# Kernel optimization log

Measured on AMD Instinct MI355X. Metric: run time of the kernel, lower is better.

The kernel has to match this reference:

```python
import jax, jax.numpy as jnp
import numpy as np

N_SAMPLES = 262144  # 2^18
DIM = 3
NUM_FLOWS = 8
HIDDEN = 64


def setup_inputs() -> dict:
    key = jax.random.key(0)
    ks = jax.random.split(key, 16)
    s = 0.05  # small param scale so exp() chains across 8 flows stay stable
    eps = jax.random.normal(ks[0], (N_SAMPLES, DIM), dtype=jnp.float32)
    L_tril = jnp.eye(DIM, dtype=jnp.float32) * np.float32(np.sqrt(0.1)) + s * jnp.tril(jax.random.normal(ks[1], (DIM, DIM), dtype=jnp.float32))
    base_mean = s * jax.random.normal(ks[2], (DIM,), dtype=jnp.float32)
    an_log_scale = s * jax.random.normal(ks[3], (NUM_FLOWS, DIM), dtype=jnp.float32)
    an_shift = s * jax.random.normal(ks[4], (NUM_FLOWS, DIM), dtype=jnp.float32)
    # permutation matrices (buffers, non-trainable)
    rng = np.random.RandomState(0)
    perm_p = np.zeros((NUM_FLOWS, DIM, DIM), dtype=np.float32)
    for i in range(NUM_FLOWS):
        perm = rng.permutation(DIM)
        perm_p[i, np.arange(DIM), perm] = 1.0
    perm_p = jnp.asarray(perm_p)
    sign_s = jnp.sign(jax.random.normal(ks[5], (NUM_FLOWS, DIM))) .astype(jnp.float32)
    sign_s = jnp.where(sign_s == 0, 1.0, sign_s)
    lu_l = s * jax.random.normal(ks[6], (NUM_FLOWS, DIM, DIM), dtype=jnp.float32)
    lu_u = s * jax.random.normal(ks[7], (NUM_FLOWS, DIM, DIM), dtype=jnp.float32)
    lu_log_s = s * jax.random.normal(ks[8], (NUM_FLOWS, DIM), dtype=jnp.float32)
    W1 = s * jax.random.normal(ks[9], (NUM_FLOWS, HIDDEN, 1), dtype=jnp.float32)
    b1 = s * jax.random.normal(ks[10], (NUM_FLOWS, HIDDEN), dtype=jnp.float32)
    W2 = s * jax.random.normal(ks[11], (NUM_FLOWS, HIDDEN, HIDDEN), dtype=jnp.float32)
    b2 = s * jax.random.normal(ks[12], (NUM_FLOWS, HIDDEN), dtype=jnp.float32)
    W3 = s * jax.random.normal(ks[13], (NUM_FLOWS, 4, HIDDEN), dtype=jnp.float32)
    b3 = s * jax.random.normal(ks[14], (NUM_FLOWS, 4), dtype=jnp.float32)
    return dict(eps=eps, L_tril=L_tril, base_mean=base_mean,
                an_log_scale=an_log_scale, an_shift=an_shift,
                perm_p=perm_p, sign_s=sign_s, lu_l=lu_l, lu_u=lu_u,
                lu_log_s=lu_log_s, W1=W1, b1=b1, W2=W2, b2=b2, W3=W3, b3=b3)


def _glow_forward(eps, L_tril, base_mean, an_log_scale, an_shift, perm_p,
                  sign_s, lu_l, lu_u, lu_log_s, W1, b1, W2, b2, W3, b3):
    eye = jnp.eye(DIM, dtype=eps.dtype)
    # base sample via Cholesky of (tril(L)+1e-6*I)(.)^T
    Lt = jnp.tril(L_tril) + eye * 1e-6
    cov = Lt @ Lt.T
    L = jnp.linalg.cholesky(cov)
    z = base_mean + eps @ L.T                      # [N, 3]
    log_det = jnp.zeros(eps.shape[0], dtype=eps.dtype)

    def step(carry, p):
        z, ld = carry
        ls, sh, P, ss, lm, um, lls, w1, bb1, w2, bb2, w3, bb3 = p
        # ActNorm
        z = jnp.exp(ls) * (z + sh)
        ld = ld + jnp.sum(ls)
        # Invertible 1x1 conv (LU parameterization)
        l = jnp.tril(lm, -1) + eye
        u = jnp.triu(um, 1)
        W = P @ l @ (u + jnp.diag(ss * jnp.exp(lls)))
        z = z @ W.T
        ld = ld + jnp.sum(lls)  # == slogdet(W)[1] since |det P|=1, det L=1
        # Affine coupling: split 1 / 2, MLP 1->64->64->4
        z1, z2 = z[:, :1], z[:, 1:]
        h = jax.nn.relu(z1 @ w1.T + bb1)
        h = jax.nn.relu(h @ w2.T + bb2)
        out = h @ w3.T + bb3                        # [N, 4]
        shift, log_scale = out[:, :2], out[:, 2:]
        z2 = z2 * jnp.exp(log_scale) + shift
        ld = ld + jnp.sum(log_scale, axis=1)
        return (jnp.concatenate([z1, z2], axis=1), ld), None

    (z, log_det), _ = jax.lax.scan(
        step, (z, log_det),
        (an_log_scale, an_shift, perm_p, sign_s, lu_l, lu_u, lu_log_s,
         W1, b1, W2, b2, W3, b3))

    # final positivity transform on columns 1, 2
    z_t = jnp.concatenate([z[:, :1], jnp.exp(z[:, 1:3])], axis=1)
    log_det = log_det + z[:, 1] + z[:, 2]
    return z_t, log_det


def reference(eps, L_tril, base_mean, an_log_scale, an_shift, perm_p, sign_s,
              lu_l, lu_u, lu_log_s, W1, b1, W2, b2, W3, b3):
    return _glow_forward(eps, L_tril, base_mean, an_log_scale, an_shift,
                         perm_p, sign_s, lu_l, lu_u, lu_log_s,
                         W1, b1, W2, b2, W3, b3)
```

## Files before the change

kernel.cpp:

```cpp
#include <hip/hip_runtime.h>
#include <hip/hip_bf16.h>

#define N_SAMPLES 262144
#define NUM_FLOWS 8
#define BLOCK 256
#define WAVES 4
#define MT 2
#define SAMPLES_PER_BLOCK (WAVES * MT * 16)
#define NBLOCKS (N_SAMPLES / SAMPLES_PER_BLOCK)

#define OFF_W1    0
#define OFF_B1    512
#define OFF_B2    1024
#define OFF_B3    1536
#define OFF_CONST 1568
#define OFF_LC    1696
#define OFF_MEAN  1708
#define OFF_LDB   1711
#define OFF_A3    1728
#define WS_PARAMS 5824
#define WS_W2_BYTE_OFF (WS_PARAMS * 4)
#define SP_FLOATS 1536

typedef __attribute__((ext_vector_type(8))) short bf16x8;
typedef __attribute__((ext_vector_type(4))) short shortx4;
typedef __attribute__((ext_vector_type(4))) float floatx4;

union FragU { bf16x8 v; __hip_bfloat162 p[4]; __hip_bfloat16 e[8]; };
union S4U   { shortx4 v; __hip_bfloat16 e[4]; };

__device__ __forceinline__ float b2f(__hip_bfloat16 x) { return __bfloat162float(x); }

__device__ __forceinline__ float ldv(const void* p, int i, bool f32) {
    return f32 ? ((const float*)p)[i] : b2f(((const __hip_bfloat16*)p)[i]);
}
__device__ __forceinline__ void stv(void* p, int i, float v, bool f32) {
    if (f32) ((float*)p)[i] = v;
    else ((__hip_bfloat16*)p)[i] = __float2bfloat16(v);
}

__global__ void prep_kernel(
    const void* __restrict__ g_L_tril,
    const void* __restrict__ g_base_mean,
    const void* __restrict__ g_an_log_scale,
    const void* __restrict__ g_an_shift,
    const void* __restrict__ g_perm_p,
    const void* __restrict__ g_sign_s,
    const void* __restrict__ g_lu_l,
    const void* __restrict__ g_lu_u,
    const void* __restrict__ g_lu_log_s,
    const void* __restrict__ g_W1,
    const void* __restrict__ g_b1,
    const void* __restrict__ g_W2,
    const void* __restrict__ g_b2,
    const void* __restrict__ g_W3,
    const void* __restrict__ g_b3,
    float* __restrict__ ws)
{
    const bool f32 = (((const float*)g_L_tril)[1] == 0.0f);
    const int f = blockIdx.x;
    const int tid = threadIdx.x;
    __hip_bfloat16* wsW2 = (__hip_bfloat16*)((char*)ws + WS_W2_BYTE_OFF);
    __hip_bfloat16* wsA3 = (__hip_bfloat16*)(ws + OFF_A3);

    if (f < NUM_FLOWS) {
        for (int i4 = tid; i4 < 1024; i4 += BLOCK) {
            int e = i4 << 2;
            int n = e >> 6, k = e & 63;
            int dst = ((k >> 5) * 4 + (n >> 4)) * 512 + (((k >> 3) & 3) * 16 + (n & 15)) * 8 + (k & 7);
            S4U u;
            if (f32) {
                float4 v = ((const float4*)g_W2)[f * 1024 + i4];
                u.e[0] = __float2bfloat16(v.x);
                u.e[1] = __float2bfloat16(v.y);
                u.e[2] = __float2bfloat16(v.z);
                u.e[3] = __float2bfloat16(v.w);
            } else {
                u.v = ((const shortx4*)g_W2)[f * 1024 + i4];
            }
            *(shortx4*)&wsW2[f * 4096 + dst] = u.v;
        }
        if (tid < 128) {
            int kc2 = tid >> 6, L = tid & 63;
            int m = L & 15, qd = L >> 4;
            FragU fr;
#pragma unroll
            for (int j = 0; j < 8; ++j) {
                int jt = ((j >> 2) << 1) | kc2;
                int r  = j & 3;
                int n  = jt * 16 + qd * 4 + r;
                fr.e[j] = __float2bfloat16(ldv(g_W3, f * 256 + (m & 3) * 64 + n, f32));
            }
            *(bf16x8*)&wsA3[(f * 2 + kc2) * 512 + L * 8] = fr.v;
        }
        if (tid < 64) {
            ws[OFF_W1 + f * 64 + tid] = ldv(g_W1, f * 64 + tid, f32);
            ws[OFF_B1 + f * 64 + tid] = ldv(g_b1, f * 64 + tid, f32);
            ws[OFF_B2 + f * 64 + tid] = ldv(g_b2, f * 64 + tid, f32);
        }
        if (tid < 4) ws[OFF_B3 + f * 4 + tid] = ldv(g_b3, f * 4 + tid, f32);
        if (tid == 0) {
            for (int d = 0; d < 3; ++d) {
                float ls = ldv(g_an_log_scale, f * 3 + d, f32);
                ws[OFF_CONST + f * 16 + 9 + d]  = __expf(ls);
                ws[OFF_CONST + f * 16 + 12 + d] = ldv(g_an_shift, f * 3 + d, f32);
            }
            float U[3][3], Lm[3][3], M[3][3], P[3][3];
            for (int i = 0; i < 3; ++i)
                for (int j = 0; j < 3; ++j) {
                    U[i][j]  = (j > i) ? ldv(g_lu_u, f * 9 + i * 3 + j, f32) : 0.f;
                    Lm[i][j] = (j < i) ? ldv(g_lu_l, f * 9 + i * 3 + j, f32) : (i == j ? 1.f : 0.f);
                    P[i][j]  = ldv(g_perm_p, f * 9 + i * 3 + j, f32);
                }
            for (int i = 0; i < 3; ++i)
                U[i][i] = ldv(g_sign_s, f * 3 + i, f32) * __expf(ldv(g_lu_log_s, f * 3 + i, f32));
            for (int i = 0; i < 3; ++i)
                for (int j = 0; j < 3; ++j) {
                    float s = 0.f;
                    for (int k = 0; k < 3; ++k) s += Lm[i][k] * U[k][j];
                    M[i][j] = s;
                }
            for (int i = 0; i < 3; ++i)
                for (int j = 0; j < 3; ++j) {
                    float s = 0.f;
                    for (int k = 0; k < 3; ++k) s += P[i][k] * M[k][j];
                    ws[OFF_CONST + f * 16 + i * 3 + j] = s;
                }
            ws[OFF_CONST + f * 16 + 15] = 0.f;
        }
    } else if (tid == 0) {
        float Lt[3][3];
        for (int i = 0; i < 3; ++i)
            for (int j = 0; j < 3; ++j)
                Lt[i][j] = (j <= i) ? ldv(g_L_tril, i * 3 + j, f32) : 0.f;
        for (int i = 0; i < 3; ++i) Lt[i][i] += 1e-6f;
        float cov[3][3];
        for (int i = 0; i < 3; ++i)
            for (int j = 0; j < 3; ++j) {
                float s = 0.f;
                for (int k = 0; k < 3; ++k) s += Lt[i][k] * Lt[j][k];
                cov[i][j] = s;
            }
        float c00 = sqrtf(cov[0][0]);
        float c10 = cov[1][0] / c00, c20 = cov[2][0] / c00;
        float c11 = sqrtf(cov[1][1] - c10 * c10);
        float c21 = (cov[2][1] - c20 * c10) / c11;
        float c22 = sqrtf(cov[2][2] - c20 * c20 - c21 * c21);
        ws[OFF_LC + 0] = c00; ws[OFF_LC + 3] = c10; ws[OFF_LC + 4] = c11;
        ws[OFF_LC + 6] = c20; ws[OFF_LC + 7] = c21; ws[OFF_LC + 8] = c22;
        ws[OFF_LC + 1] = 0.f; ws[OFF_LC + 2] = 0.f; ws[OFF_LC + 5] = 0.f;
        ws[OFF_LC + 9] = 0.f; ws[OFF_LC + 10] = 0.f; ws[OFF_LC + 11] = 0.f;
        for (int d = 0; d < 3; ++d) ws[OFF_MEAN + d] = ldv(g_base_mean, d, f32);
        float ldb = 0.f;
        for (int i = 0; i < NUM_FLOWS * 3; ++i)
            ldb += ldv(g_an_log_scale, i, f32) + ldv(g_lu_log_s, i, f32);
        ws[OFF_LDB] = ldb;
    }
}

__global__ __launch_bounds__(BLOCK, 2) void glow_kernel(
    const void* __restrict__ g_eps,
    const void* __restrict__ g_L_tril,
    const float* __restrict__ ws,
    void* __restrict__ g_out)
{
    const bool f32 = (((const float*)g_L_tril)[1] == 0.0f);

    __shared__ __align__(16) float sP[SP_FLOATS];
    for (int i = threadIdx.x; i < SP_FLOATS / 4; i += BLOCK)
        ((float4*)sP)[i] = ((const float4*)ws)[i];
    __syncthreads();

    const __hip_bfloat16* wsW2 = (const __hip_bfloat16*)((const char*)ws + WS_W2_BYTE_OFF);
    const __hip_bfloat16* wsA3 = (const __hip_bfloat16*)(ws + OFF_A3);

    const int tid  = threadIdx.x;
    const int lane = tid & 63;
    const int wave = tid >> 6;
    const int quad = lane >> 4;
    const int col  = lane & 15;
    const int base = blockIdx.x * SAMPLES_PER_BLOCK + wave * (MT * 16);

    float zc0[MT], zc1[MT], zc2[MT], lda[MT];
    {
        const float l00 = ws[OFF_LC + 0], l10 = ws[OFF_LC + 3], l11 = ws[OFF_LC + 4];
        const float l20 = ws[OFF_LC + 6], l21 = ws[OFF_LC + 7], l22 = ws[OFF_LC + 8];
        const float m0 = ws[OFF_MEAN], m1 = ws[OFF_MEAN + 1], m2 = ws[OFF_MEAN + 2];
#pragma unroll
        for (int mt = 0; mt < MT; ++mt) {
            int g = base + mt * 16 + col;
            float e0 = ldv(g_eps, g * 3 + 0, f32);
            float e1 = ldv(g_eps, g * 3 + 1, f32);
            float e2 = ldv(g_eps, g * 3 + 2, f32);
            zc0[mt] = m0 + l00 * e0;
            zc1[mt] = m1 + l10 * e0 + l11 * e1;
            zc2[mt] = m2 + l20 * e0 + l21 * e1 + l22 * e2;
            lda[mt] = 0.f;
        }
    }

#pragma unroll 1
    for (int f = 0; f < NUM_FLOWS; ++f) {
        bf16x8 Af[2][4];
#pragma unroll
        for (int kc = 0; kc < 2; ++kc)
#pragma unroll
            for (int jt = 0; jt < 4; ++jt)
                Af[kc][jt] = *(const bf16x8*)&wsW2[f * 4096 + ((kc * 4 + jt) * 64 + lane) * 8];
        bf16x8 A3f[2];
#pragma unroll
        for (int kc2 = 0; kc2 < 2; ++kc2)
            A3f[kc2] = *(const bf16x8*)&wsA3[((f * 2 + kc2) * 64 + lane) * 8];

        floatx4 b2q[4];
#pragma unroll
        for (int jt = 0; jt < 4; ++jt)
            b2q[jt] = *(const floatx4*)&sP[OFF_B2 + f * 64 + jt * 16 + quad * 4];

        const floatx4* cp = (const floatx4*)&ws[OFF_CONST + f * 16];
        floatx4 c0 = cp[0], c1 = cp[1], c2 = cp[2], c3 = cp[3];
        floatx4 b3v = *(const floatx4*)&ws[OFF_B3 + f * 4];

#pragma unroll
        for (int mt = 0; mt < MT; ++mt) {
            float t0 = c2[1] * (zc0[mt] + c3[0]);
            float t1 = c2[2] * (zc1[mt] + c3[1]);
            float t2 = c2[3] * (zc2[mt] + c3[2]);
            zc0[mt] = c0[0] * t0 + c0[1] * t1 + c0[2] * t2;
            zc1[mt] = c0[3] * t0 + c1[0] * t1 + c1[1] * t2;
            zc2[mt] = c1[2] * t0 + c1[3] * t1 + c2[0] * t2;
        }

        FragU hB[MT][2];
#pragma unroll
        for (int kc = 0; kc < 2; ++kc) {
            const floatx4* w1p = (const floatx4*)&sP[OFF_W1 + f * 64 + kc * 32 + quad * 8];
            const floatx4* b1p = (const floatx4*)&sP[OFF_B1 + f * 64 + kc * 32 + quad * 8];
            floatx4 w1a = w1p[0], w1b = w1p[1];
            floatx4 b1a = b1p[0], b1b = b1p[1];
#pragma unroll
            for (int mt = 0; mt < MT; ++mt) {
                float z0 = zc0[mt];
#pragma unroll
                for (int w = 0; w < 2; ++w) {
                    float a0 = fmaxf(fmaf(z0, w1a[2 * w],     b1a[2 * w]),     0.f);
                    float a1 = fmaxf(fmaf(z0, w1a[2 * w + 1], b1a[2 * w + 1]), 0.f);
                    float b0 = fmaxf(fmaf(z0, w1b[2 * w],     b1b[2 * w]),     0.f);
                    float b1 = fmaxf(fmaf(z0, w1b[2 * w + 1], b1b[2 * w + 1]), 0.f);
                    hB[mt][kc].p[w]     = __float22bfloat162_rn(make_float2(a0, a1));
                    hB[mt][kc].p[2 + w] = __float22bfloat162_rn(make_float2(b0, b1));
                }
            }
        }

#pragma unroll
        for (int mt = 0; mt < MT; ++mt) {
            floatx4 a2[4];
#pragma unroll
            for (int jt = 0; jt < 4; ++jt) {
                floatx4 acc = __builtin_amdgcn_mfma_f32_16x16x32_bf16(Af[0][jt], hB[mt][0].v, b2q[jt], 0, 0, 0);
                a2[jt] = __builtin_amdgcn_mfma_f32_16x16x32_bf16(Af[1][jt], hB[mt][1].v, acc, 0, 0, 0);
            }
            FragU h3[2];
#pragma unroll
            for (int jt = 0; jt < 4; ++jt) {
                int kc2 = jt & 1, pb = (jt >> 1) * 2;
                h3[kc2].p[pb]     = __float22bfloat162_rn(make_float2(fmaxf(a2[jt][0], 0.f), fmaxf(a2[jt][1], 0.f)));
                h3[kc2].p[pb + 1] = __float22bfloat162_rn(make_float2(fmaxf(a2[jt][2], 0.f), fmaxf(a2[jt][3], 0.f)));
            }
            floatx4 acc3 = {0.f, 0.f, 0.f, 0.f};
            acc3 = __builtin_amdgcn_mfma_f32_16x16x32_bf16(A3f[0], h3[0].v, acc3, 0, 0, 0);
            acc3 = __builtin_amdgcn_mfma_f32_16x16x32_bf16(A3f[1], h3[1].v, acc3, 0, 0, 0);
            float sh0 = acc3[0] + b3v[0];
            float sh1 = acc3[1] + b3v[1];
            float ls0 = acc3[2] + b3v[2];
            float ls1 = acc3[3] + b3v[3];
            zc1[mt] = fmaf(zc1[mt], __expf(ls0), sh0);
            zc2[mt] = fmaf(zc2[mt], __expf(ls1), sh1);
            lda[mt] += ls0 + ls1;
        }
    }

    if (quad == 0) {
        const float ldBase = ws[OFF_LDB];
#pragma unroll
        for (int mt = 0; mt < MT; ++mt) {
            int g = base + mt * 16 + col;
            float z1 = zc1[mt], z2 = zc2[mt];
            stv(g_out, g * 3 + 0, zc0[mt], f32);
            stv(g_out, g * 3 + 1, __expf(z1), f32);
            stv(g_out, g * 3 + 2, __expf(z2), f32);
            stv(g_out, 3 * N_SAMPLES + g, lda[mt] + ldBase + z1 + z2, f32);
        }
    }
}

extern "C" void kernel_launch(void* const* d_in, const int* in_sizes, int n_in,
                              void* d_out, int out_size, void* d_ws, size_t ws_size,
                              hipStream_t stream) {
    prep_kernel<<<dim3(NUM_FLOWS + 1), dim3(BLOCK), 0, stream>>>(
        d_in[1], d_in[2], d_in[3], d_in[4], d_in[5], d_in[6], d_in[7],
        d_in[8], d_in[9], d_in[10], d_in[11], d_in[12], d_in[13], d_in[14], d_in[15],
        (float*)d_ws);
    glow_kernel<<<dim3(NBLOCKS), dim3(BLOCK), 0, stream>>>(
        d_in[0], d_in[1], (const float*)d_ws, d_out);
}
```

Baseline: 129.3 us.

## Prefetch next flow's MFMA fragments and compute first layer in packed bf16

The flow loop is restructured into a two-stage software pipeline that loads the next flow's W2/W3 MFMA fragments from global memory while the current flow computes, hiding load latency. W1 and b1 are now stored as bf16 in shared memory, and the first MLP layer uses packed bf16 hfma2/hmax2 instead of fp32 FMAs plus conversions. The b3 bias is folded into the MFMA accumulator init. This costs extra registers for the double-buffered fragments and reduces the first layer's precision to bf16.

```diff
diff --git a/kernel.cpp b/kernel.cpp
--- a/kernel.cpp
+++ b/kernel.cpp
@@ -9,18 +9,18 @@
 #define SAMPLES_PER_BLOCK (WAVES * MT * 16)
 #define NBLOCKS (N_SAMPLES / SAMPLES_PER_BLOCK)
 
-#define OFF_W1    0
-#define OFF_B1    512
-#define OFF_B2    1024
-#define OFF_B3    1536
-#define OFF_CONST 1568
-#define OFF_LC    1696
-#define OFF_MEAN  1708
-#define OFF_LDB   1711
-#define OFF_A3    1728
-#define WS_PARAMS 5824
+#define OFF_B2    0
+#define OFF_W1B   512
+#define OFF_B1B   768
+#define SP_FLOATS 1024
+#define OFF_B3    1024
+#define OFF_CONST 1056
+#define OFF_LC    1184
+#define OFF_MEAN  1196
+#define OFF_LDB   1199
+#define OFF_A3    1200
+#define WS_PARAMS 5296
 #define WS_W2_BYTE_OFF (WS_PARAMS * 4)
-#define SP_FLOATS 1536
 
 typedef __attribute__((ext_vector_type(8))) short bf16x8;
 typedef __attribute__((ext_vector_type(4))) short shortx4;
@@ -60,8 +60,10 @@
     const bool f32 = (((const float*)g_L_tril)[1] == 0.0f);
     const int f = blockIdx.x;
     const int tid = threadIdx.x;
-    __hip_bfloat16* wsW2 = (__hip_bfloat16*)((char*)ws + WS_W2_BYTE_OFF);
-    __hip_bfloat16* wsA3 = (__hip_bfloat16*)(ws + OFF_A3);
+    __hip_bfloat16* wsW2  = (__hip_bfloat16*)((char*)ws + WS_W2_BYTE_OFF);
+    __hip_bfloat16* wsA3  = (__hip_bfloat16*)(ws + OFF_A3);
+    __hip_bfloat16* wsW1b = (__hip_bfloat16*)(ws + OFF_W1B);
+    __hip_bfloat16* wsB1b = (__hip_bfloat16*)(ws + OFF_B1B);
 
     if (f < NUM_FLOWS) {
         for (int i4 = tid; i4 < 1024; i4 += BLOCK) {
@@ -94,8 +96,8 @@
             *(bf16x8*)&wsA3[(f * 2 + kc2) * 512 + L * 8] = fr.v;
         }
         if (tid < 64) {
-            ws[OFF_W1 + f * 64 + tid] = ldv(g_W1, f * 64 + tid, f32);
-            ws[OFF_B1 + f * 64 + tid] = ldv(g_b1, f * 64 + tid, f32);
+            wsW1b[f * 64 + tid] = __float2bfloat16(ldv(g_W1, f * 64 + tid, f32));
+            wsB1b[f * 64 + tid] = __float2bfloat16(ldv(g_b1, f * 64 + tid, f32));
             ws[OFF_B2 + f * 64 + tid] = ldv(g_b2, f * 64 + tid, f32);
         }
         if (tid < 4) ws[OFF_B3 + f * 4 + tid] = ldv(g_b3, f * 4 + tid, f32);
@@ -158,6 +160,11 @@
     }
 }
 
+struct Frags {
+    bf16x8 Af[2][4];
+    bf16x8 A3f[2];
+};
+
 __global__ __launch_bounds__(BLOCK, 2) void glow_kernel(
     const void* __restrict__ g_eps,
     const void* __restrict__ g_L_tril,
@@ -171,8 +178,10 @@
         ((float4*)sP)[i] = ((const float4*)ws)[i];
     __syncthreads();
 
-    const __hip_bfloat16* wsW2 = (const __hip_bfloat16*)((const char*)ws + WS_W2_BYTE_OFF);
-    const __hip_bfloat16* wsA3 = (const __hip_bfloat16*)(ws + OFF_A3);
+    const __hip_bfloat16* wsW2  = (const __hip_bfloat16*)((const char*)ws + WS_W2_BYTE_OFF);
+    const __hip_bfloat16* wsA3  = (const __hip_bfloat16*)(ws + OFF_A3);
+    const __hip_bfloat16* sW1b  = (const __hip_bfloat16*)(sP + OFF_W1B);
+    const __hip_bfloat16* sB1b  = (const __hip_bfloat16*)(sP + OFF_B1B);
 
     const int tid  = threadIdx.x;
     const int lane = tid & 63;
@@ -199,19 +208,23 @@
         }
     }
 
-#pragma unroll 1
-    for (int f = 0; f < NUM_FLOWS; ++f) {
-        bf16x8 Af[2][4];
+    __hip_bfloat162 zero2;
+    zero2.x = __float2bfloat16(0.f); zero2.y = zero2.x;
+
+    auto loadFrags = [&](int f) {
+        Frags fr;
 #pragma unroll
         for (int kc = 0; kc < 2; ++kc)
 #pragma unroll
             for (int jt = 0; jt < 4; ++jt)
-                Af[kc][jt] = *(const bf16x8*)&wsW2[f * 4096 + ((kc * 4 + jt) * 64 + lane) * 8];
-        bf16x8 A3f[2];
+                fr.Af[kc][jt] = *(const bf16x8*)&wsW2[f * 4096 + ((kc * 4 + jt) * 64 + lane) * 8];
 #pragma unroll
         for (int kc2 = 0; kc2 < 2; ++kc2)
-            A3f[kc2] = *(const bf16x8*)&wsA3[((f * 2 + kc2) * 64 + lane) * 8];
-
+            fr.A3f[kc2] = *(const bf16x8*)&wsA3[((f * 2 + kc2) * 64 + lane) * 8];
+        return fr;
+    };
+
+    auto flowBody = [&](int f, const Frags& fr) {
         floatx4 b2q[4];
 #pragma unroll
         for (int jt = 0; jt < 4; ++jt)
@@ -232,25 +245,22 @@
         }
 
         FragU hB[MT][2];
+        __hip_bfloat162 z02[MT];
+#pragma unroll
+        for (int mt = 0; mt < MT; ++mt) {
+            __hip_bfloat16 zb = __float2bfloat16(zc0[mt]);
+            z02[mt].x = zb; z02[mt].y = zb;
+        }
 #pragma unroll
         for (int kc = 0; kc < 2; ++kc) {
-            const floatx4* w1p = (const floatx4*)&sP[OFF_W1 + f * 64 + kc * 32 + quad * 8];
-            const floatx4* b1p = (const floatx4*)&sP[OFF_B1 + f * 64 + kc * 32 + quad * 8];
-            floatx4 w1a = w1p[0], w1b = w1p[1];
-            floatx4 b1a = b1p[0], b1b = b1p[1];
-#pragma unroll
-            for (int mt = 0; mt < MT; ++mt) {
-                float z0 = zc0[mt];
-#pragma unroll
-                for (int w = 0; w < 2; ++w) {
-                    float a0 = fmaxf(fmaf(z0, w1a[2 * w],     b1a[2 * w]),     0.f);
-                    float a1 = fmaxf(fmaf(z0, w1a[2 * w + 1], b1a[2 * w + 1]), 0.f);
-                    float b0 = fmaxf(fmaf(z0, w1b[2 * w],     b1b[2 * w]),     0.f);
-                    float b1 = fmaxf(fmaf(z0, w1b[2 * w + 1], b1b[2 * w + 1]), 0.f);
-                    hB[mt][kc].p[w]     = __float22bfloat162_rn(make_float2(a0, a1));
-                    hB[mt][kc].p[2 + w] = __float22bfloat162_rn(make_float2(b0, b1));
-                }
-            }
+            FragU w1u, b1u;
+            w1u.v = *(const bf16x8*)&sW1b[f * 64 + kc * 32 + quad * 8];
+            b1u.v = *(const bf16x8*)&sB1b[f * 64 + kc * 32 + quad * 8];
+#pragma unroll
+            for (int mt = 0; mt < MT; ++mt)
+#pragma unroll
+                for (int i = 0; i < 4; ++i)
+                    hB[mt][kc].p[i] = __hmax2(__hfma2(z02[mt], w1u.p[i], b1u.p[i]), zero2);
         }
 
 #pragma unroll
@@ -258,8 +268,8 @@
             floatx4 a2[4];
 #pragma unroll
             for (int jt = 0; jt < 4; ++jt) {
-                floatx4 acc = __builtin_amdgcn_mfma_f32_16x16x32_bf16(Af[0][jt], hB[mt][0].v, b2q[jt], 0, 0, 0);
-                a2[jt] = __builtin_amdgcn_mfma_f32_16x16x32_bf16(Af[1][jt], hB[mt][1].v, acc, 0, 0, 0);
+                floatx4 acc = __builtin_amdgcn_mfma_f32_16x16x32_bf16(fr.Af[0][jt], hB[mt][0].v, b2q[jt], 0, 0, 0);
+                a2[jt] = __builtin_amdgcn_mfma_f32_16x16x32_bf16(fr.Af[1][jt], hB[mt][1].v, acc, 0, 0, 0);
             }
             FragU h3[2];
 #pragma unroll
@@ -268,17 +278,23 @@
                 h3[kc2].p[pb]     = __float22bfloat162_rn(make_float2(fmaxf(a2[jt][0], 0.f), fmaxf(a2[jt][1], 0.f)));
                 h3[kc2].p[pb + 1] = __float22bfloat162_rn(make_float2(fmaxf(a2[jt][2], 0.f), fmaxf(a2[jt][3], 0.f)));
             }
-            floatx4 acc3 = {0.f, 0.f, 0.f, 0.f};
-            acc3 = __builtin_amdgcn_mfma_f32_16x16x32_bf16(A3f[0], h3[0].v, acc3, 0, 0, 0);
-            acc3 = __builtin_amdgcn_mfma_f32_16x16x32_bf16(A3f[1], h3[1].v, acc3, 0, 0, 0);
-            float sh0 = acc3[0] + b3v[0];
-            float sh1 = acc3[1] + b3v[1];
-            float ls0 = acc3[2] + b3v[2];
-            float ls1 = acc3[3] + b3v[3];
-            zc1[mt] = fmaf(zc1[mt], __expf(ls0), sh0);
-            zc2[mt] = fmaf(zc2[mt], __expf(ls1), sh1);
+            floatx4 acc3 = b3v;
+            acc3 = __builtin_amdgcn_mfma_f32_16x16x32_bf16(fr.A3f[0], h3[0].v, acc3, 0, 0, 0);
+            acc3 = __builtin_amdgcn_mfma_f32_16x16x32_bf16(fr.A3f[1], h3[1].v, acc3, 0, 0, 0);
+            float ls0 = acc3[2], ls1 = acc3[3];
+            zc1[mt] = fmaf(zc1[mt], __expf(ls0), acc3[0]);
+            zc2[mt] = fmaf(zc2[mt], __expf(ls1), acc3[1]);
             lda[mt] += ls0 + ls1;
         }
+    };
+
+    Frags A = loadFrags(0);
+#pragma unroll 1
+    for (int fb = 0; fb < NUM_FLOWS; fb += 2) {
+        Frags B = loadFrags(fb + 1);
+        flowBody(fb, A);
+        A = loadFrags(fb + 2 < NUM_FLOWS ? fb + 2 : NUM_FLOWS - 1);
+        flowBody(fb + 1, B);
     }
 
     if (quad == 0) {
```

Result: slower. 139.7 us (+8.0%).
